# Optimization experiments

Hardware: AMD Instinct MI355X
Metric: run time of the kernel (lower is better)

The kernel has to match this reference:

```python
import jax, jax.numpy as jnp
import numpy as np

B, N, E, H, D = 8, 1024, 512, 8, 64  # batch, tokens, embed, heads, dim_head


def setup_inputs() -> dict:
    key = jax.random.key(0)
    ks = jax.random.split(key, 12)
    f = lambda k, s: jax.random.normal(k, s, dtype=jnp.float32)
    return {
        "x": f(ks[0], (B, N, E)),
        "r_t": f(ks[1], (B, N, E)),
        "r_c": f(ks[2], (B, N, E)),
        "bias_time_e": f(ks[3], (H, D)) * 0.02,
        "bias_time_r": f(ks[4], (H, D)) * 0.02,
        "bias_channel_r": f(ks[5], (H, D)) * 0.02,
        "bias_channel_e": f(ks[6], (H, D)) * 0.02,
        "w_qkv": f(ks[7], (E, 3 * H * D)) * 0.02,   # to_qkv (no bias)
        "w_kr_t": f(ks[8], (E, H * D)) * 0.02,      # k_r_time_net (no bias)
        "w_kr_c": f(ks[9], (E, H * D)) * 0.02,      # k_r_channel_net (no bias)
        "w_out": f(ks[10], (H * D, E)) * 0.02,      # to_out Linear
        "b_out": f(ks[11], (E,)) * 0.02,
    }


def _rel_shift(x):
    # x: [i, j, b, h] -- TransformerXL relative shift along j
    i, j, b, h = x.shape
    zp = jnp.zeros((i, 1, b, h), x.dtype)
    xp = jnp.concatenate([zp, x], axis=1).reshape(j + 1, i, b, h)
    return xp[1:].reshape(i, j, b, h)


def reference(x, r_t, r_c, bias_time_e, bias_time_r, bias_channel_r, bias_channel_e,
              w_qkv, w_kr_t, w_kr_c, w_out, b_out):
    b, n, _ = x.shape
    to_nbhd = lambda t: t.reshape(b, n, H, D).transpose(1, 0, 2, 3)  # [n,b,h,d]
    q, k, v = jnp.split(x @ w_qkv, 3, axis=-1)
    q, k, v = to_nbhd(q), to_nbhd(k), to_nbhd(v)
    qb = q + bias_time_e  # broadcast [h,d] over [n,b,h,d]
    wr_t = to_nbhd(r_t @ w_kr_t)
    wr_c = to_nbhd(r_c @ w_kr_c)
    AC = jnp.einsum('ibhd,jbhd->ijbh', qb, k)
    BD_t = _rel_shift(jnp.einsum('ibhd,jbhd->ijbh', qb, wr_t))
    BD_c = _rel_shift(jnp.einsum('ibhd,jbhd->ijbh', qb, wr_c))
    dots = AC + (BD_t + BD_c) * 0.5
    # Faithful to torch: nn.Softmax(dim=-1) on [i,j,b,h] normalizes over HEADS.
    attn = jax.nn.softmax(dots, axis=-1)
    out = jnp.einsum('ijbh,jbhd->ibhd', attn, v)
    out = out.transpose(1, 0, 2, 3).reshape(b, n, H * D) @ w_out + b_out
    return out, attn.transpose(2, 3, 0, 1)  # ([b,n,E], [b,h,q,k])
```

## Files before the change

kernel.cpp:

```cpp
#include <hip/hip_runtime.h>
#include <hip/hip_fp16.h>


typedef _Float16 f16;
typedef f16 f16x4 __attribute__((ext_vector_type(4)));
typedef f16 f16x8 __attribute__((ext_vector_type(8)));
typedef float f32x4 __attribute__((ext_vector_type(4)));

#define MFMA16(a,b,c) __builtin_amdgcn_mfma_f32_16x16x32_f16((a),(b),(c),0,0,0)

static __device__ __forceinline__ size_t qpidx(int bh, int q, int d) {
  return ((((size_t)bh * 64 + (q >> 4)) * 2 + (d >> 5)) * 64 +
          ((q & 15) + (((d >> 3) & 3) << 4))) * 8 + (d & 7);
}
static __device__ __forceinline__ size_t vpidx(int bh, int d, int j) {
  return ((((size_t)bh * 4 + (d >> 4)) * 32 + (j >> 5)) * 64 +
          ((d & 15) + (((j >> 3) & 3) << 4))) * 8 + (j & 7);
}

__global__ __launch_bounds__(256) void kprep(
    const float* __restrict__ x, const float* __restrict__ rt, const float* __restrict__ rc,
    const float* __restrict__ wqkv, const float* __restrict__ wkrt, const float* __restrict__ wkrc,
    f16* __restrict__ X16, f16* __restrict__ A2, f16* __restrict__ WQ, f16* __restrict__ W2)
{
  const int t = threadIdx.x, gx = blockIdx.x, mode = blockIdx.y;
  if (mode <= 2) {
    const size_t id = (size_t)gx * 256 + t;
    const float* src = (mode == 0) ? x : (mode == 1) ? rt : rc;
    float4 v0 = *(const float4*)&src[id * 8];
    float4 v1 = *(const float4*)&src[id * 8 + 4];
    f16x8 o = {(f16)v0.x, (f16)v0.y, (f16)v0.z, (f16)v0.w,
               (f16)v1.x, (f16)v1.y, (f16)v1.z, (f16)v1.w};
    if (mode == 0) *(f16x8*)&X16[id * 8] = o;
    else {
      const int mrow = (int)(id >> 6), cc = (int)(id & 63);
      *(f16x8*)&A2[(size_t)mrow * 1024 + (mode == 2 ? 512 : 0) + cc * 8] = o;
    }
  } else if (mode == 3) {
    if (gx >= 384) return;
    const int c = gx & 63, n = (gx >> 6) * 256 + t;
    f16x8 o;
    #pragma unroll
    for (int e = 0; e < 8; ++e) o[e] = (f16)wqkv[(size_t)(c * 8 + e) * 1536 + n];
    *(f16x8*)&WQ[(size_t)n * 512 + c * 8] = o;
  } else {
    if (gx >= 128) return;
    const int c = gx & 63, n = (gx >> 6) * 256 + t;
    const float* src = (mode == 4) ? wkrt : wkrc;
    f16x8 o;
    #pragma unroll
    for (int e = 0; e < 8; ++e) o[e] = (f16)src[(size_t)(c * 8 + e) * 512 + n];
    *(f16x8*)&W2[(size_t)n * 1024 + (mode == 5 ? 512 : 0) + c * 8] = o;
  }
}

__global__ __launch_bounds__(256) void kproj(
    const f16* __restrict__ X16, const f16* __restrict__ A2,
    const f16* __restrict__ WQ, const f16* __restrict__ W2,
    const float* __restrict__ bias_te,
    f16* __restrict__ QP, f16* __restrict__ KP, f16* __restrict__ VP, f16* __restrict__ WP)
{
  __shared__ f16 As[128 * 64];
  __shared__ f16 Bs[128 * 64];
  const int t = threadIdx.x, l = t & 63, w = t >> 6;
  const int wr = w >> 1, wc = w & 1;
  const int lin = blockIdx.x + 64 * blockIdx.y;
  const int mchunk = lin & 7;
  const int rem = lin >> 3;
  const int m0 = (mchunk * 8 + (rem & 7)) * 128;
  const int y = rem >> 3;
  const int mode = y >> 2;
  const bool wrs = (mode == 3);
  const f16* Asrc = wrs ? A2 : X16;
  const int lda = wrs ? 1024 : 512;
  const int K = wrs ? 1024 : 512;
  const f16* Bsrc = wrs ? (W2 + (size_t)((y - 12) * 128) * 1024)
                        : (WQ + (size_t)(y * 128) * 512);
  const int ldb = wrs ? 1024 : 512;

  f32x4 acc[4][4] = {};
  for (int k0 = 0; k0 < K; k0 += 64) {
    __syncthreads();
    #pragma unroll
    for (int rep = 0; rep < 4; ++rep) {
      const int idx = rep * 256 + t;
      const int row = idx >> 3, kb = idx & 7;
      const int slot = (kb ^ (row & 7)) << 3;
      f16x8 va = *(const f16x8*)&Asrc[(size_t)(m0 + row) * lda + k0 + kb * 8];
      *(f16x8*)&As[row * 64 + slot] = va;
      f16x8 vb = *(const f16x8*)&Bsrc[(size_t)row * ldb + k0 + kb * 8];
      *(f16x8*)&Bs[row * 64 + slot] = vb;
    }
    __syncthreads();
    #pragma unroll
    for (int kc = 0; kc < 2; ++kc) {
      f16x8 af[4], bf[4];
      const int kb = kc * 4 + (l >> 4);
      #pragma unroll
      for (int mb = 0; mb < 4; ++mb) {
        const int r = wr * 64 + mb * 16 + (l & 15);
        af[mb] = *(const f16x8*)&As[r * 64 + ((kb ^ (r & 7)) << 3)];
      }
      #pragma unroll
      for (int nb = 0; nb < 4; ++nb) {
        const int r = wc * 64 + nb * 16 + (l & 15);
        bf[nb] = *(const f16x8*)&Bs[r * 64 + ((kb ^ (r & 7)) << 3)];
      }
      #pragma unroll
      for (int mb = 0; mb < 4; ++mb)
      #pragma unroll
      for (int nb = 0; nb < 4; ++nb)
        acc[mb][nb] = MFMA16(af[mb], bf[nb], acc[mb][nb]);
    }
  }
  #pragma unroll
  for (int mb = 0; mb < 4; ++mb)
  #pragma unroll
  for (int nb = 0; nb < 4; ++nb) {
    const int loc = wc * 64 + nb * 16 + (l & 15);
    const int c = (y & 3) * 128 + loc;
    const int hh = c >> 6, d = c & 63;
    const float badd = (mode == 0) ? bias_te[c] : 0.f;
    f32x4 a = acc[mb][nb];
    #pragma unroll
    for (int r = 0; r < 4; ++r) {
      const int m = m0 + wr * 64 + mb * 16 + (l >> 4) * 4 + r;
      const int bb = m >> 10, tn = m & 1023;
      const int bh = bb * 8 + hh;
      const float v = a[r] + badd;
      if (mode == 0)      QP[qpidx(bh, tn, d)] = (f16)v;
      else if (mode == 1) KP[qpidx(bh, tn, d)] = (f16)v;
      else if (mode == 2) VP[vpidx(bh, d, tn)] = (f16)v;
      else                WP[qpidx(bh, tn, d)] = (f16)(0.5f * v);
    }
  }
}

__global__ __launch_bounds__(512, 4) void kdots(
    const f16* __restrict__ QP, const f16* __restrict__ KP,
    const f16* __restrict__ WP, const f16* __restrict__ VP,
    float* __restrict__ attn_out, f16* __restrict__ OUTP)
{
  __shared__ f16 sd[8][32][72];
  const int t = threadIdx.x, l = t & 63, h = t >> 6;
  const int lin = blockIdx.x + 4 * blockIdx.y + 128 * blockIdx.z;
  const int b = lin & 7;
  const int rem = lin >> 3;
  const int kg = rem & 3;
  const int q0 = (rem >> 2) * 32;
  const int bh = b * 8 + h;
  const f16x8* QP8 = (const f16x8*)QP;
  const f16x8* KP8 = (const f16x8*)KP;
  const f16x8* WP8 = (const f16x8*)WP;
  const f16x8* VP8 = (const f16x8*)VP;
  const int qrow = (l >> 4) * 4;
  f16x8 aq[3][2];
  #pragma unroll
  for (int mb = 0; mb < 3; ++mb)
  #pragma unroll
  for (int kc = 0; kc < 2; ++kc)
    aq[mb][kc] = QP8[((size_t)(bh * 64 + (q0 >> 4) + mb) * 2 + kc) * 64 + l];

  f32x4 oacc[2][4] = {};

  for (int kti = 0; kti < 4; ++kti) {
    const int k0 = (kg * 4 + kti) * 64;
    const int u0 = k0 - q0;
    auto rawblockT = [&](int jb) {
      f32x4 racc[3] = {};
      #pragma unroll
      for (int kc = 0; kc < 2; ++kc) {
        f16x8 wf = WP8[((size_t)(bh * 64 + jb) * 2 + kc) * 64 + l];
        #pragma unroll
        for (int qb = 0; qb < 3; ++qb)
          racc[qb] = MFMA16(wf, aq[qb][kc], racc[qb]);
      }
      #pragma unroll
      for (int qb = 0; qb < 3; ++qb) {
        const int qloc = qb * 16 + (l & 15);
        const int base = (q0 + qloc) + (jb * 16 + qrow) - 1023;
        #pragma unroll
        for (int r = 0; r < 4; ++r) {
          int kd = base + r;
          int row = qloc;
          if (kd < k0) { kd += 1024; row -= 1; }
          if ((unsigned)row < 32u && (unsigned)(kd - k0) < 64u)
            sd[h][row][kd - k0] = (f16)racc[qb][r];
        }
      }
    };
    {
      const int blo_e = u0 - 33, bhi_e = (u0 + 61 > 1023) ? 1023 : u0 + 61;
      if (bhi_e >= 0) {
        const int blo = (blo_e < 0 ? 0 : blo_e) >> 4, bhi = bhi_e >> 4;
        for (int jb = blo; jb <= bhi; ++jb) rawblockT(jb);
      }
      if (u0 <= 31) {
        const int alo_e = 992 + u0, ahi_e = (1086 + u0 > 1023) ? 1023 : 1086 + u0;
        const int alo = (alo_e < 0 ? 0 : alo_e) >> 4, ahi = ahi_e >> 4;
        for (int jb = alo; jb <= ahi; ++jb) rawblockT(jb);
      }
    }
    {
      f32x4 acc[4][2] = {};
      #pragma unroll
      for (int kc = 0; kc < 2; ++kc) {
        #pragma unroll
        for (int kb = 0; kb < 4; ++kb) {
          f16x8 kf = KP8[((size_t)(bh * 64 + (k0 >> 4) + kb) * 2 + kc) * 64 + l];
          #pragma unroll
          for (int qb = 0; qb < 2; ++qb)
            acc[kb][qb] = MFMA16(kf, aq[qb][kc], acc[kb][qb]);
        }
      }
      #pragma unroll
      for (int kb = 0; kb < 4; ++kb)
      #pragma unroll
      for (int qb = 0; qb < 2; ++qb) {
        const int qloc = qb * 16 + (l & 15);
        const int kbase = kb * 16 + qrow;
        const int hol = (q0 + qloc + 1) - (k0 + kbase);
        f16x4 cur = *(const f16x4*)&sd[h][qloc][kbase];
        f16x4 res;
        #pragma unroll
        for (int e = 0; e < 4; ++e) {
          const float rv = (e == hol) ? 0.f : (float)cur[e];
          res[e] = (f16)(rv + acc[kb][qb][e]);
        }
        *(f16x4*)&sd[h][qloc][kbase] = res;
      }
    }
    __syncthreads();
    {
      const int o = t * 4, q = o >> 6, k = o & 63;
      float dv[8][4];
      #pragma unroll
      for (int hh = 0; hh < 8; ++hh) {
        f16x4 v = *(const f16x4*)&sd[hh][q][k];
        dv[hh][0] = (float)v[0]; dv[hh][1] = (float)v[1];
        dv[hh][2] = (float)v[2]; dv[hh][3] = (float)v[3];
      }
      #pragma unroll
      for (int e = 0; e < 4; ++e) {
        float m = dv[0][e];
        #pragma unroll
        for (int hh = 1; hh < 8; ++hh) m = fmaxf(m, dv[hh][e]);
        float ssum = 0.f;
        #pragma unroll
        for (int hh = 0; hh < 8; ++hh) { float a = __expf(dv[hh][e] - m); dv[hh][e] = a; ssum += a; }
        float rinv = 1.f / ssum;
        #pragma unroll
        for (int hh = 0; hh < 8; ++hh) dv[hh][e] *= rinv;
      }
      const size_t qg = q0 + q;
      #pragma unroll
      for (int hh = 0; hh < 8; ++hh) {
        f32x4* dst = (f32x4*)&attn_out[((size_t)(b * 8 + hh) * 1024 + qg) * 1024 + k0 + k];
        __builtin_nontemporal_store(f32x4{dv[hh][0], dv[hh][1], dv[hh][2], dv[hh][3]}, dst);
        *(f16x4*)&sd[hh][q][k] =
            f16x4{(f16)dv[hh][0], (f16)dv[hh][1], (f16)dv[hh][2], (f16)dv[hh][3]};
      }
    }
    __syncthreads();
    #pragma unroll
    for (int kc = 0; kc < 2; ++kc) {
      f16x8 pa[2];
      #pragma unroll
      for (int mb = 0; mb < 2; ++mb) {
        const int qq = mb * 16 + (l & 15);
        const int jj = kc * 32 + (l >> 4) * 8;
        pa[mb] = *(const f16x8*)&sd[h][qq][jj];
      }
      #pragma unroll
      for (int nb = 0; nb < 4; ++nb) {
        f16x8 vb = VP8[(((size_t)bh * 4 + nb) * 32 + (k0 >> 5) + kc) * 64 + l];
        #pragma unroll
        for (int mb = 0; mb < 2; ++mb)
          oacc[mb][nb] = MFMA16(pa[mb], vb, oacc[mb][nb]);
      }
    }
  }
  f16* op = OUTP + ((size_t)kg * 8192 + (size_t)b * 1024) * 512;
  #pragma unroll
  for (int mb = 0; mb < 2; ++mb)
  #pragma unroll
  for (int nb = 0; nb < 4; ++nb)
  #pragma unroll
  for (int r = 0; r < 4; ++r) {
    const int qg = q0 + mb * 16 + qrow + r;
    const int dd = nb * 16 + (l & 15);
    op[(size_t)qg * 512 + h * 64 + dd] = (f16)oacc[mb][nb][r];
  }
}

__global__ __launch_bounds__(256) void kout(
    const f16* __restrict__ OUTP, const float* __restrict__ w_out,
    const float* __restrict__ b_out, float* __restrict__ out)
{
  __shared__ f16 a_s[128][36];
  __shared__ f16 b_s[64][36];
  const int t = threadIdx.x, l = t & 63, w = t >> 6;
  const int m0 = blockIdx.x * 128;
  const int c0 = blockIdx.y * 64;
  f32x4 acc[2][4] = {};
  for (int k0 = 0; k0 < 512; k0 += 32) {
    __syncthreads();
    #pragma unroll
    for (int rep = 0; rep < 2; ++rep) {
      const int s = rep * 256 + t;
      const int r = s >> 2, c = (s & 3) * 8;
      const size_t off = (size_t)(m0 + r) * 512 + k0 + c;
      f16x8 p0 = *(const f16x8*)&OUTP[off];
      f16x8 p1 = *(const f16x8*)&OUTP[off + 4194304];
      f16x8 p2 = *(const f16x8*)&OUTP[off + 8388608];
      f16x8 p3 = *(const f16x8*)&OUTP[off + 12582912];
      f16x4 lo, hi;
      #pragma unroll
      for (int e = 0; e < 4; ++e) {
        lo[e] = (f16)((float)p0[e] + (float)p1[e] + (float)p2[e] + (float)p3[e]);
        hi[e] = (f16)((float)p0[e+4] + (float)p1[e+4] + (float)p2[e+4] + (float)p3[e+4]);
      }
      *(f16x4*)&a_s[r][c]     = lo;
      *(f16x4*)&a_s[r][c + 4] = hi;
    }
    #pragma unroll
    for (int rep = 0; rep < 2; ++rep) {
      int idx = rep * 1024 + t * 4;
      int kr = idx >> 6, c = idx & 63;
      float4 v = *(const float4*)&w_out[(size_t)(k0 + kr) * 512 + c0 + c];
      b_s[c + 0][kr] = (f16)v.x; b_s[c + 1][kr] = (f16)v.y;
      b_s[c + 2][kr] = (f16)v.z; b_s[c + 3][kr] = (f16)v.w;
    }
    __syncthreads();
    const int kc = (l >> 4) * 8;
    f16x8 af[2];
    #pragma unroll
    for (int mb = 0; mb < 2; ++mb) {
      int r = w * 32 + mb * 16 + (l & 15);
      af[mb] = __builtin_shufflevector(*(const f16x4*)&a_s[r][kc], *(const f16x4*)&a_s[r][kc + 4],
                                       0, 1, 2, 3, 4, 5, 6, 7);
    }
    #pragma unroll
    for (int nb = 0; nb < 4; ++nb) {
      int cc = nb * 16 + (l & 15);
      f16x8 bf = __builtin_shufflevector(*(const f16x4*)&b_s[cc][kc], *(const f16x4*)&b_s[cc][kc + 4],
                                         0, 1, 2, 3, 4, 5, 6, 7);
      #pragma unroll
      for (int mb = 0; mb < 2; ++mb)
        acc[mb][nb] = MFMA16(af[mb], bf, acc[mb][nb]);
    }
  }
  #pragma unroll
  for (int mb = 0; mb < 2; ++mb)
  #pragma unroll
  for (int nb = 0; nb < 4; ++nb) {
    const int cg = c0 + nb * 16 + (l & 15);
    const float bb = b_out[cg];
    #pragma unroll
    for (int r = 0; r < 4; ++r) {
      const int m = m0 + w * 32 + mb * 16 + (l >> 4) * 4 + r;
      out[(size_t)m * 512 + cg] = acc[mb][nb][r] + bb;
    }
  }
}

extern "C" void kernel_launch(void* const* d_in, const int* in_sizes, int n_in,
                              void* d_out, int out_size, void* d_ws, size_t ws_size,
                              hipStream_t stream) {
  const float* x       = (const float*)d_in[0];
  const float* rt      = (const float*)d_in[1];
  const float* rc      = (const float*)d_in[2];
  const float* bias_te = (const float*)d_in[3];
  const float* w_qkv   = (const float*)d_in[7];
  const float* w_kr_t  = (const float*)d_in[8];
  const float* w_kr_c  = (const float*)d_in[9];
  const float* w_out   = (const float*)d_in[10];
  const float* b_out   = (const float*)d_in[11];
  float* out = (float*)d_out;
  float* attn_out = out + (size_t)8 * 1024 * 512;

  const size_t oX16 = 0;
  const size_t oA2  = oX16 + 4194304;
  const size_t oWQ  = oA2  + 8388608;
  const size_t oW2  = oWQ  + 786432;
  const size_t oQP  = oW2  + 524288;
  const size_t oKP  = oQP  + 4194304;
  const size_t oVP  = oKP  + 4194304;
  const size_t oWP  = oVP  + 4194304;
  const size_t oOP  = oWP  + 4194304;
  const size_t NEEDED = (oOP + (size_t)4 * 8192 * 512) * 2;
  if (ws_size < NEEDED) return;
  f16* ws = (f16*)d_ws;
  f16 *X16 = ws + oX16, *A2 = ws + oA2, *WQ = ws + oWQ, *W2 = ws + oW2;
  f16 *QP = ws + oQP, *KP = ws + oKP, *VP = ws + oVP, *WP = ws + oWP;
  f16* OUTP = ws + oOP;

  kprep<<<dim3(2048, 6), 256, 0, stream>>>(x, rt, rc, w_qkv, w_kr_t, w_kr_c,
                                           X16, A2, WQ, W2);
  kproj<<<dim3(64, 16), 256, 0, stream>>>(X16, A2, WQ, W2, bias_te, QP, KP, VP, WP);
  kdots<<<dim3(4, 32, 8), 512, 0, stream>>>(QP, KP, WP, VP, attn_out, OUTP);
  kout<<<dim3(64, 8), 256, 0, stream>>>(OUTP, w_out, b_out, out);
}
```

Before: 230.4 us.

## Process 128-wide key tiles with XOR-swizzled LDS and skip unneeded rel-shift MFMAs

The attention-dots kernel now walks two 128-key tiles per block instead of four 64-key tiles. This halves the number of barrier rounds and cuts the overlap in redundant relative-position blocks recomputed at tile edges. The shared score buffer grows to 128 columns and uses an XOR swizzle on the column index to avoid LDS bank conflicts in place of padding. The wrap-around rel-shift blocks skip the third q-block MFMA they do not need. The larger LDS footprint (64KB per block) may reduce occupancy against the launch bound of 4 blocks.

```diff
diff --git a/kernel.cpp b/kernel.cpp
--- a/kernel.cpp
+++ b/kernel.cpp
@@ -141,7 +141,7 @@
     const f16* __restrict__ WP, const f16* __restrict__ VP,
     float* __restrict__ attn_out, f16* __restrict__ OUTP)
 {
-  __shared__ f16 sd[8][32][72];
+  __shared__ f16 sd[8][32][128];
   const int t = threadIdx.x, l = t & 63, h = t >> 6;
   const int lin = blockIdx.x + 4 * blockIdx.y + 128 * blockIdx.z;
   const int b = lin & 7;
@@ -163,80 +163,89 @@
 
   f32x4 oacc[2][4] = {};
 
-  for (int kti = 0; kti < 4; ++kti) {
-    const int k0 = (kg * 4 + kti) * 64;
-    const int u0 = k0 - q0;
-    auto rawblockT = [&](int jb) {
+  #pragma unroll 1
+  for (int pr = 0; pr < 2; ++pr) {
+    const int pk0 = kg * 256 + pr * 128;
+    const int u = pk0 - q0;
+    auto rawblockT = [&](int jb, bool q2) {
       f32x4 racc[3] = {};
       #pragma unroll
       for (int kc = 0; kc < 2; ++kc) {
         f16x8 wf = WP8[((size_t)(bh * 64 + jb) * 2 + kc) * 64 + l];
-        #pragma unroll
-        for (int qb = 0; qb < 3; ++qb)
-          racc[qb] = MFMA16(wf, aq[qb][kc], racc[qb]);
+        racc[0] = MFMA16(wf, aq[0][kc], racc[0]);
+        racc[1] = MFMA16(wf, aq[1][kc], racc[1]);
+        if (q2) racc[2] = MFMA16(wf, aq[2][kc], racc[2]);
       }
       #pragma unroll
       for (int qb = 0; qb < 3; ++qb) {
+        if (qb == 2 && !q2) break;
         const int qloc = qb * 16 + (l & 15);
         const int base = (q0 + qloc) + (jb * 16 + qrow) - 1023;
         #pragma unroll
         for (int r = 0; r < 4; ++r) {
           int kd = base + r;
           int row = qloc;
-          if (kd < k0) { kd += 1024; row -= 1; }
-          if ((unsigned)row < 32u && (unsigned)(kd - k0) < 64u)
-            sd[h][row][kd - k0] = (f16)racc[qb][r];
+          if (kd < pk0) { kd += 1024; row -= 1; }
+          const unsigned col = (unsigned)(kd - pk0);
+          if ((unsigned)row < 32u && col < 128u)
+            sd[h][row][col ^ ((row & 7) << 3)] = (f16)racc[qb][r];
         }
       }
     };
     {
-      const int blo_e = u0 - 33, bhi_e = (u0 + 61 > 1023) ? 1023 : u0 + 61;
+      const int bhi_e = (u + 126 > 1023) ? 1023 : u + 126;
       if (bhi_e >= 0) {
+        const int blo_e = u - 33;
         const int blo = (blo_e < 0 ? 0 : blo_e) >> 4, bhi = bhi_e >> 4;
-        for (int jb = blo; jb <= bhi; ++jb) rawblockT(jb);
-      }
-      if (u0 <= 31) {
-        const int alo_e = 992 + u0, ahi_e = (1086 + u0 > 1023) ? 1023 : 1086 + u0;
-        const int alo = (alo_e < 0 ? 0 : alo_e) >> 4, ahi = ahi_e >> 4;
-        for (int jb = alo; jb <= ahi; ++jb) rawblockT(jb);
-      }
-    }
-    {
+        for (int jb = blo; jb <= bhi; ++jb) rawblockT(jb, true);
+      }
+    }
+    if (u <= 31) {
+      const int alo_e = 992 + u;
+      const int ahi_e = (1150 + u > 1023) ? 1023 : 1150 + u;
+      const int alo = (alo_e < 0 ? 0 : alo_e) >> 4, ahi = ahi_e >> 4;
+      for (int jb = alo; jb <= ahi; ++jb) rawblockT(jb, false);
+    }
+    #pragma unroll
+    for (int sub = 0; sub < 2; ++sub) {
       f32x4 acc[4][2] = {};
-      #pragma unroll
-      for (int kc = 0; kc < 2; ++kc) {
-        #pragma unroll
-        for (int kb = 0; kb < 4; ++kb) {
-          f16x8 kf = KP8[((size_t)(bh * 64 + (k0 >> 4) + kb) * 2 + kc) * 64 + l];
-          #pragma unroll
-          for (int qb = 0; qb < 2; ++qb)
-            acc[kb][qb] = MFMA16(kf, aq[qb][kc], acc[kb][qb]);
-        }
+      const int kk = (pk0 >> 4) + sub * 4;
+      #pragma unroll
+      for (int kc = 0; kc < 2; ++kc)
+      #pragma unroll
+      for (int kb = 0; kb < 4; ++kb) {
+        f16x8 kf = KP8[((size_t)(bh * 64 + kk + kb) * 2 + kc) * 64 + l];
+        acc[kb][0] = MFMA16(kf, aq[0][kc], acc[kb][0]);
+        acc[kb][1] = MFMA16(kf, aq[1][kc], acc[kb][1]);
       }
       #pragma unroll
       for (int kb = 0; kb < 4; ++kb)
       #pragma unroll
       for (int qb = 0; qb < 2; ++qb) {
         const int qloc = qb * 16 + (l & 15);
-        const int kbase = kb * 16 + qrow;
-        const int hol = (q0 + qloc + 1) - (k0 + kbase);
-        f16x4 cur = *(const f16x4*)&sd[h][qloc][kbase];
+        const int kbase = sub * 64 + kb * 16 + qrow;
+        const int hol = (q0 + qloc + 1) - (pk0 + kbase);
+        f16* p = &sd[h][qloc][kbase ^ ((qloc & 7) << 3)];
+        f16x4 cur = *(const f16x4*)p;
         f16x4 res;
         #pragma unroll
         for (int e = 0; e < 4; ++e) {
           const float rv = (e == hol) ? 0.f : (float)cur[e];
           res[e] = (f16)(rv + acc[kb][qb][e]);
         }
-        *(f16x4*)&sd[h][qloc][kbase] = res;
-      }
-    }
-    __syncthreads();
-    {
-      const int o = t * 4, q = o >> 6, k = o & 63;
+        *(f16x4*)p = res;
+      }
+    }
+    __syncthreads();
+    #pragma unroll
+    for (int pass = 0; pass < 2; ++pass) {
+      const int idx = pass * 2048 + t * 4;
+      const int q = idx >> 7, k = idx & 127;
+      const int ks = k ^ ((q & 7) << 3);
       float dv[8][4];
       #pragma unroll
       for (int hh = 0; hh < 8; ++hh) {
-        f16x4 v = *(const f16x4*)&sd[hh][q][k];
+        f16x4 v = *(const f16x4*)&sd[hh][q][ks];
         dv[hh][0] = (float)v[0]; dv[hh][1] = (float)v[1];
         dv[hh][2] = (float)v[2]; dv[hh][3] = (float)v[3];
       }
@@ -255,25 +264,25 @@
       const size_t qg = q0 + q;
       #pragma unroll
       for (int hh = 0; hh < 8; ++hh) {
-        f32x4* dst = (f32x4*)&attn_out[((size_t)(b * 8 + hh) * 1024 + qg) * 1024 + k0 + k];
+        f32x4* dst = (f32x4*)&attn_out[((size_t)(b * 8 + hh) * 1024 + qg) * 1024 + pk0 + k];
         __builtin_nontemporal_store(f32x4{dv[hh][0], dv[hh][1], dv[hh][2], dv[hh][3]}, dst);
-        *(f16x4*)&sd[hh][q][k] =
+        *(f16x4*)&sd[hh][q][ks] =
             f16x4{(f16)dv[hh][0], (f16)dv[hh][1], (f16)dv[hh][2], (f16)dv[hh][3]};
       }
     }
     __syncthreads();
     #pragma unroll
-    for (int kc = 0; kc < 2; ++kc) {
+    for (int kc = 0; kc < 4; ++kc) {
       f16x8 pa[2];
       #pragma unroll
       for (int mb = 0; mb < 2; ++mb) {
         const int qq = mb * 16 + (l & 15);
         const int jj = kc * 32 + (l >> 4) * 8;
-        pa[mb] = *(const f16x8*)&sd[h][qq][jj];
+        pa[mb] = *(const f16x8*)&sd[h][qq][jj ^ ((qq & 7) << 3)];
       }
       #pragma unroll
       for (int nb = 0; nb < 4; ++nb) {
-        f16x8 vb = VP8[(((size_t)bh * 4 + nb) * 32 + (k0 >> 5) + kc) * 64 + l];
+        f16x8 vb = VP8[(((size_t)bh * 4 + nb) * 32 + (pk0 >> 5) + kc) * 64 + l];
         #pragma unroll
         for (int mb = 0; mb < 2; ++mb)
           oacc[mb][nb] = MFMA16(pa[mb], vb, oacc[mb][nb]);
```

Result: slower. 240.6 us (+4.4%).
